# Kernel optimization log

Hardware: AMD Instinct MI355X
Metric: run time of the kernel (lower is better)

The kernel has to match this reference:

```python
import jax, jax.numpy as jnp
import numpy as np

N, C = 8192, 64

def setup_inputs() -> dict:
    key = jax.random.key(0)
    k1, k2, k3 = jax.random.split(key, 3)
    values = jax.random.normal(k1, (N, C), dtype=jnp.float32)
    coords = jax.random.uniform(k2, (N, 2), dtype=jnp.float32)
    spacing = jax.random.uniform(k3, (2,), dtype=jnp.float32)
    shift = jnp.zeros((2,), dtype=jnp.float32)
    return {"values": values, "coords": coords, "spacing": spacing, "shift": shift}


def reference(values, coords, spacing, shift):
    # grid_mode branch of upsample_nn: 3 shifted copies of the coord grid
    x, y = coords[:, 0], coords[:, 1]
    new_coords = jnp.concatenate([
        jnp.stack((x + spacing[0], y + spacing[1]), axis=1),
        jnp.stack((x, y + spacing[1]), axis=1),
        jnp.stack((x + spacing[0], y), axis=1),
    ], axis=0)  # [3N, 2]

    # Diffs = ||(new_coords - shift)[:,None] - coords[None,:]||, argmin over coords.
    # argmin of the L2 norm == argmin of the squared distance, so use the
    # expanded form to avoid materializing the [3N, N, 2] difference tensor.
    a = new_coords - shift  # [3N, 2]
    d2 = (jnp.sum(a * a, axis=1)[:, None]
          + jnp.sum(coords * coords, axis=1)[None, :]
          - 2.0 * a @ coords.T)  # [3N, N]
    idx = jnp.argmin(d2, axis=1)  # [3N]
    new_values = values[idx]      # [3N, C]

    out_values = jnp.concatenate([values, new_values], axis=0)   # [4N, C]
    out_coords = jnp.concatenate([coords, new_coords], axis=0)   # [4N, 2]
    return out_values, out_coords
```

## Files before the change

kernel.cpp:

```cpp
#include <hip/hip_runtime.h>

#pragma clang fp contract(off)

#define N_PTS 8192
#define C_DIM 64
#define NQ (3 * N_PTS)
#define G 64
#define NCELL (G * G)
#define MARGIN 1.2e-5f
#define HCELL (1.0f / 64.0f)
#define QBLOCKS (NQ / 32)
#define STRIPEBLKS 16
#define CPS (NCELL / STRIPEBLKS)
#define COPYBLKS 128


__device__ __forceinline__ unsigned int fsortkey(float f) {
    const unsigned int u = __float_as_uint(f);
    return (u & 0x80000000u) ? ~u : (u | 0x80000000u);
}
__device__ __forceinline__ float finvkey(unsigned int e) {
    const unsigned int u = (e & 0x80000000u) ? (e & 0x7fffffffu) : ~e;
    return __uint_as_float(u);
}

__device__ __forceinline__ void shift_query(int g, float x, float y,
                                            float sx, float sy,
                                            float& nx, float& ny) {
    if (g == 0)      { nx = x + sx; ny = y + sy; }
    else if (g == 1) { nx = x;      ny = y + sy; }
    else             { nx = x + sx; ny = y; }
}

__global__ __launch_bounds__(1024) void build_copy_kernel(
    const float2* __restrict__ coords2,
    const float4* __restrict__ values4,
    float4* __restrict__ sorted,
    int* __restrict__ starts,
    float4* __restrict__ out_values4,
    float2* __restrict__ out_coords)
{
#pragma clang fp contract(off)
    const int t = threadIdx.x;
    if (blockIdx.x >= STRIPEBLKS) {
        const int row = ((int)blockIdx.x - STRIPEBLKS) * 64 + (t >> 4);
        const int c4  = t & 15;
        out_values4[row * 16 + c4] = values4[row * 16 + c4];
        if (c4 == 0) out_coords[row] = coords2[row];
        return;
    }

    __shared__ unsigned int lhist[CPS];
    __shared__ unsigned int wred[16];
    __shared__ unsigned int wsum2[4];
    __shared__ unsigned int baseSh;

    const int b      = blockIdx.x;
    const int myBase = b * CPS;
    const int lane   = t & 63;
    const int w      = t >> 6;

    if (t < CPS) lhist[t] = 0u;
    __syncthreads();

    float2 cpt[8];
    int    cell[8];
    int cnt = 0;
    #pragma unroll
    for (int k = 0; k < 8; ++k) {
        const int i = t + 1024 * k;
        const float2 c = coords2[i];
        cpt[k] = c;
        int cx = (int)(c.x * 64.0f); cx = min(max(cx, 0), G - 1);
        int cy = (int)(c.y * 64.0f); cy = min(max(cy, 0), G - 1);
        cell[k] = cy * G + cx;
        cnt += (cell[k] < myBase) ? 1 : 0;
        const int lc = cell[k] - myBase;
        if (lc >= 0 && lc < CPS) atomicAdd(&lhist[lc], 1u);
    }

    int cv = cnt;
    #pragma unroll
    for (int s = 32; s >= 1; s >>= 1) cv += __shfl_xor(cv, s, 64);
    if (lane == 0) wred[w] = (unsigned)cv;
    __syncthreads();
    if (t == 0) {
        unsigned s = 0;
        #pragma unroll
        for (int j = 0; j < 16; ++j) s += wred[j];
        baseSh = s;
    }
    __syncthreads();
    const unsigned base = baseSh;

    unsigned h = 0, v = 0;
    if (t < CPS) {
        h = lhist[t];
        v = h;
        #pragma unroll
        for (int s = 1; s < 64; s <<= 1) {
            const unsigned o = __shfl_up(v, s, 64);
            if (lane >= s) v += o;
        }
        if (lane == 63) wsum2[w] = v;
    }
    __syncthreads();
    if (t < CPS) {
        unsigned woff = 0;
        for (int j = 0; j < w; ++j) woff += wsum2[j];
        const unsigned excl = base + woff + v - h;
        starts[myBase + t] = (int)excl;
        lhist[t] = excl;
    }
    if (b == 0 && t == 0) starts[NCELL] = N_PTS;
    __syncthreads();

    #pragma unroll
    for (int k = 0; k < 8; ++k) {
        const int lc = cell[k] - myBase;
        if (lc >= 0 && lc < CPS) {
            const unsigned pos = atomicAdd(&lhist[lc], 1u);
            const float p0 = cpt[k].x * cpt[k].x;
            const float p1 = cpt[k].y * cpt[k].y;
            const float sc = p0 + p1;
            const int i = t + 1024 * k;
            sorted[pos] = make_float4(cpt[k].x, cpt[k].y, sc, __int_as_float(i));
        }
    }
}

__global__ __launch_bounds__(256) void query_kernel(
    const float4* __restrict__ sorted,
    const int* __restrict__ starts,
    const float4* __restrict__ values4,
    const float* __restrict__ spacing,
    const float* __restrict__ shift,
    float4* __restrict__ out_values4,
    float2* __restrict__ out_coords)
{
#pragma clang fp contract(off)
    __shared__ int s_starts[NCELL + 1];

    const int tid  = threadIdx.x;
    const int lane = tid & 7;
    const int q    = blockIdx.x * 32 + (tid >> 3);
    const int g    = q >> 13;
    const int k    = q & (N_PTS - 1);

    const float4 me = sorted[k];

    for (int i = tid; i <= NCELL; i += 256) s_starts[i] = starts[i];

    const int b = __float_as_int(me.w);
    float nx, ny;
    shift_query(g, me.x, me.y, spacing[0], spacing[1], nx, ny);
    const float ax = nx - shift[0];
    const float ay = ny - shift[1];
    const float sa = (ax * ax) + (ay * ay);

    int cx = (int)floorf(ax * 64.0f); cx = min(max(cx, 0), G - 1);
    int cy = (int)floorf(ay * 64.0f); cy = min(max(cy, 0), G - 1);
    const float dxo = fmaxf(fmaxf(ax - 1.0f, -ax), 0.0f);

    __syncthreads();

    float best = INFINITY;
    int   bi   = 0x7fffffff;

#define EVAL_BODY(PT)                                                       \
    {                                                                       \
        const float4 pt = (PT);                                             \
        const float p   = ax * pt.x;                                        \
        const float dv  = __builtin_fmaf(ay, pt.y, p);                      \
        const float t1  = sa + pt.z;                                        \
        const float d2  = t1 - (2.0f * dv);                                 \
        const int   j   = __float_as_int(pt.w);                             \
        if (d2 < best || (d2 == best && j < bi)) { best = d2; bi = j; }     \
    }

    const int xa = max(cx - 1, 0), xb = min(cx + 1, G - 1);
    const int ya = max(cy - 1, 0), yb = min(cy + 1, G - 1);

    const int s0 = s_starts[ya * G + xa];
    const int e0 = s_starts[ya * G + xb + 1];
    int s1 = 0, e1 = 0, s2 = 0, e2 = 0;
    if (ya + 1 <= yb) { s1 = s_starts[(ya + 1) * G + xa]; e1 = s_starts[(ya + 1) * G + xb + 1]; }
    if (ya + 2 <= yb) { s2 = s_starts[(ya + 2) * G + xa]; e2 = s_starts[(ya + 2) * G + xb + 1]; }
    const int l0 = e0 - s0, l1 = e1 - s1;
    const int total = l0 + l1 + (e2 - s2);

    {
        const int i0 = lane, i1 = lane + 8, i2 = lane + 16;
        const bool v0 = i0 < total, v1 = i1 < total, v2 = i2 < total;
        float4 p0, p1, p2;
        int a0 = 0, a1 = 0, a2 = 0;
        if (v0) a0 = (i0 < l0) ? s0 + i0 : ((i0 < l0 + l1) ? s1 + (i0 - l0) : s2 + (i0 - l0 - l1));
        if (v1) a1 = (i1 < l0) ? s0 + i1 : ((i1 < l0 + l1) ? s1 + (i1 - l0) : s2 + (i1 - l0 - l1));
        if (v2) a2 = (i2 < l0) ? s0 + i2 : ((i2 < l0 + l1) ? s1 + (i2 - l0) : s2 + (i2 - l0 - l1));
        if (v0) p0 = sorted[a0];
        if (v1) p1 = sorted[a1];
        if (v2) p2 = sorted[a2];
        if (v0) EVAL_BODY(p0)
        if (v1) EVAL_BODY(p1)
        if (v2) EVAL_BODY(p2)
        for (int idx = lane + 24; idx < total; idx += 8) {
            const int a = (idx < l0) ? s0 + idx
                        : ((idx < l0 + l1) ? s1 + (idx - l0) : s2 + (idx - l0 - l1));
            EVAL_BODY(sorted[a])
        }
    }

    unsigned long long key =
        ((unsigned long long)fsortkey(best) << 32) | (unsigned int)bi;
    #pragma unroll
    for (int m = 1; m < 8; m <<= 1) {
        const unsigned long long o = __shfl_xor(key, m, 8);
        if (o < key) key = o;
    }
    best = finvkey((unsigned int)(key >> 32));
    bi   = (int)(unsigned int)key;

    const float U = best + MARGIN;

    float sr = sqrtf(fmaxf(U - dxo * dxo, 0.0f));
    sr = fminf(sr, 4.0f);
    const int ylo = max((int)floorf((ay - sr) * 64.0f), 0);
    const int yhi = min((int)floorf((ay + sr) * 64.0f), G - 1);

    float scw = fminf(sqrtf(U), 4.0f);
    const int xlo_c = max((int)floorf((ax - scw) * 64.0f), 0);
    const int xhi_c = min((int)floorf((ax + scw) * 64.0f), G - 1);

    const bool skip = (ylo >= ya) && (yhi <= yb) && (xlo_c >= xa) && (xhi_c <= xb);

    if (!skip) {
        for (int yy = ylo; yy <= yhi; yy += 2) {
            int ssA = 0, eeA = 0, ssB = 0, eeB = 0;
            {
                const float ry0 = (float)yy * HCELL;
                const float vy  = fmaxf(fmaxf(ay - ry0 - HCELL, ry0 - ay), 0.0f);
                const float r2  = U - vy * vy;
                if (r2 >= 0.0f) {
                    const float s = fminf(sqrtf(r2), 4.0f);
                    const int xl = max((int)floorf((ax - s) * 64.0f), 0);
                    const int xh = min((int)floorf((ax + s) * 64.0f), G - 1);
                    if (xl <= xh && !(yy >= ya && yy <= yb && xl >= xa && xh <= xb)) {
                        ssA = s_starts[yy * G + xl];
                        eeA = s_starts[yy * G + xh + 1];
                    }
                }
            }
            if (yy + 1 <= yhi) {
                const int y2 = yy + 1;
                const float ry0 = (float)y2 * HCELL;
                const float vy  = fmaxf(fmaxf(ay - ry0 - HCELL, ry0 - ay), 0.0f);
                const float r2  = U - vy * vy;
                if (r2 >= 0.0f) {
                    const float s = fminf(sqrtf(r2), 4.0f);
                    const int xl = max((int)floorf((ax - s) * 64.0f), 0);
                    const int xh = min((int)floorf((ax + s) * 64.0f), G - 1);
                    if (xl <= xh && !(y2 >= ya && y2 <= yb && xl >= xa && xh <= xb)) {
                        ssB = s_starts[y2 * G + xl];
                        eeB = s_starts[y2 * G + xh + 1];
                    }
                }
            }
            const int iA = ssA + lane, iB = ssB + lane;
            const bool vA = iA < eeA, vB = iB < eeB;
            float4 pA, pB;
            if (vA) pA = sorted[iA];
            if (vB) pB = sorted[iB];
            if (vA) EVAL_BODY(pA)
            if (vB) EVAL_BODY(pB)
            for (int i = ssA + lane + 8; i < eeA; i += 8) EVAL_BODY(sorted[i])
            for (int i = ssB + lane + 8; i < eeB; i += 8) EVAL_BODY(sorted[i])
        }
        key = ((unsigned long long)fsortkey(best) << 32) | (unsigned int)bi;
        #pragma unroll
        for (int m = 1; m < 8; m <<= 1) {
            const unsigned long long o = __shfl_xor(key, m, 8);
            if (o < key) key = o;
        }
        bi = (int)(unsigned int)key;
    }
#undef EVAL_BODY

    bi = min(max(bi, 0), N_PTS - 1);
    const int qi  = g * N_PTS + b;
    const int row = N_PTS + qi;
    out_values4[row * 16 + 2 * lane + 0] = values4[bi * 16 + 2 * lane + 0];
    out_values4[row * 16 + 2 * lane + 1] = values4[bi * 16 + 2 * lane + 1];
    if (lane == 0) out_coords[row] = make_float2(nx, ny);
}

extern "C" void kernel_launch(void* const* d_in, const int* in_sizes, int n_in,
                              void* d_out, int out_size, void* d_ws, size_t ws_size,
                              hipStream_t stream)
{
    const float* values  = (const float*)d_in[0];
    const float* coords  = (const float*)d_in[1];
    const float* spacing = (const float*)d_in[2];
    const float* shift   = (const float*)d_in[3];

    float* out_values = (float*)d_out;
    float2* out_coords = (float2*)(out_values + (size_t)4 * N_PTS * C_DIM);

    char* ws = (char*)d_ws;
    float4* sorted = (float4*)ws;
    int* starts    = (int*)(ws + 131072);

    build_copy_kernel<<<STRIPEBLKS + COPYBLKS, 1024, 0, stream>>>(
        (const float2*)coords, (const float4*)values,
        sorted, starts, (float4*)out_values, out_coords);

    query_kernel<<<QBLOCKS, 256, 0, stream>>>(
        sorted, starts, (const float4*)values, spacing, shift,
        (float4*)out_values, out_coords);
}
```

Measured before the change: 23.00 us.

## Add column/row edge strips for contiguous fallback scans of out-of-grid queries

Builds two extra sorted strips in the build kernel: points in the last four grid columns binned by row, and points in the last four grid rows binned by column. Queries whose fallback search window lies entirely in those edge columns or rows (typical for shifted queries past the unit square) now scan one contiguous range instead of looping over many grid rows with per-row bounds. This targets the costly fallback loop for boundary queries, at the price of two extra build blocks, more workspace, and extra shared-memory loads.

```diff
diff --git a/kernel.cpp b/kernel.cpp
--- a/kernel.cpp
+++ b/kernel.cpp
@@ -6,6 +6,7 @@
 #define C_DIM 64
 #define NQ (3 * N_PTS)
 #define G 64
+#define GSTRIP 60
 #define NCELL (G * G)
 #define MARGIN 1.2e-5f
 #define HCELL (1.0f / 64.0f)
@@ -37,16 +38,75 @@
     const float4* __restrict__ values4,
     float4* __restrict__ sorted,
     int* __restrict__ starts,
+    int* __restrict__ cs_starts,
+    int* __restrict__ rs_starts,
+    float4* __restrict__ cstrip,
+    float4* __restrict__ rstrip,
     float4* __restrict__ out_values4,
     float2* __restrict__ out_coords)
 {
 #pragma clang fp contract(off)
     const int t = threadIdx.x;
-    if (blockIdx.x >= STRIPEBLKS) {
-        const int row = ((int)blockIdx.x - STRIPEBLKS) * 64 + (t >> 4);
+
+    if (blockIdx.x >= STRIPEBLKS + 2) {
+        const int row = ((int)blockIdx.x - STRIPEBLKS - 2) * 64 + (t >> 4);
         const int c4  = t & 15;
         out_values4[row * 16 + c4] = values4[row * 16 + c4];
         if (c4 == 0) out_coords[row] = coords2[row];
+        return;
+    }
+
+    if (blockIdx.x >= STRIPEBLKS) {
+        const bool isCol = (blockIdx.x == STRIPEBLKS);
+        int* __restrict__ sst       = isCol ? cs_starts : rs_starts;
+        float4* __restrict__ strip  = isCol ? cstrip    : rstrip;
+
+        __shared__ unsigned int shist[G];
+        if (t < G) shist[t] = 0u;
+        __syncthreads();
+
+        float2 cpt[8];
+        int    bin[8];
+        bool   inq[8];
+        #pragma unroll
+        for (int k = 0; k < 8; ++k) {
+            const int i = t + 1024 * k;
+            const float2 c = coords2[i];
+            cpt[k] = c;
+            int cx = (int)(c.x * 64.0f); cx = min(max(cx, 0), G - 1);
+            int cy = (int)(c.y * 64.0f); cy = min(max(cy, 0), G - 1);
+            inq[k] = isCol ? (cx >= GSTRIP) : (cy >= GSTRIP);
+            bin[k] = isCol ? cy : cx;
+            if (inq[k]) atomicAdd(&shist[bin[k]], 1u);
+        }
+        __syncthreads();
+
+        if (t < G) {
+            const unsigned h = shist[t];
+            unsigned v = h;
+            #pragma unroll
+            for (int s = 1; s < 64; s <<= 1) {
+                const unsigned o = __shfl_up(v, s, 64);
+                if (t >= s) v += o;
+            }
+            const unsigned excl = v - h;
+            sst[t]   = (int)excl;
+            shist[t] = excl;
+            if (t == 63) sst[G] = (int)v;
+        }
+        __syncthreads();
+
+        #pragma unroll
+        for (int k = 0; k < 8; ++k) {
+            if (inq[k]) {
+                const unsigned pos = atomicAdd(&shist[bin[k]], 1u);
+                const float p0 = cpt[k].x * cpt[k].x;
+                const float p1 = cpt[k].y * cpt[k].y;
+                const float sc = p0 + p1;
+                const int i = t + 1024 * k;
+                strip[pos] = make_float4(cpt[k].x, cpt[k].y, sc, __int_as_float(i));
+            }
+        }
         return;
     }
 
@@ -132,6 +192,10 @@
 __global__ __launch_bounds__(256) void query_kernel(
     const float4* __restrict__ sorted,
     const int* __restrict__ starts,
+    const int* __restrict__ cs_starts,
+    const int* __restrict__ rs_starts,
+    const float4* __restrict__ cstrip,
+    const float4* __restrict__ rstrip,
     const float4* __restrict__ values4,
     const float* __restrict__ spacing,
     const float* __restrict__ shift,
@@ -140,6 +204,7 @@
 {
 #pragma clang fp contract(off)
     __shared__ int s_starts[NCELL + 1];
+    __shared__ int s_cs[G + 1], s_rs[G + 1];
 
     const int tid  = threadIdx.x;
     const int lane = tid & 7;
@@ -150,6 +215,8 @@
     const float4 me = sorted[k];
 
     for (int i = tid; i <= NCELL; i += 256) s_starts[i] = starts[i];
+    if (tid < G + 1)                      s_cs[tid]       = cs_starts[tid];
+    else if (tid >= 128 && tid < 128 + G + 1) s_rs[tid - 128] = rs_starts[tid - 128];
 
     const int b = __float_as_int(me.w);
     float nx, ny;
@@ -234,46 +301,56 @@
     const bool skip = (ylo >= ya) && (yhi <= yb) && (xlo_c >= xa) && (xhi_c <= xb);
 
     if (!skip) {
-        for (int yy = ylo; yy <= yhi; yy += 2) {
-            int ssA = 0, eeA = 0, ssB = 0, eeB = 0;
-            {
-                const float ry0 = (float)yy * HCELL;
-                const float vy  = fmaxf(fmaxf(ay - ry0 - HCELL, ry0 - ay), 0.0f);
-                const float r2  = U - vy * vy;
-                if (r2 >= 0.0f) {
-                    const float s = fminf(sqrtf(r2), 4.0f);
-                    const int xl = max((int)floorf((ax - s) * 64.0f), 0);
-                    const int xh = min((int)floorf((ax + s) * 64.0f), G - 1);
-                    if (xl <= xh && !(yy >= ya && yy <= yb && xl >= xa && xh <= xb)) {
-                        ssA = s_starts[yy * G + xl];
-                        eeA = s_starts[yy * G + xh + 1];
+        if (xlo_c >= GSTRIP) {
+            const int ss = s_cs[ylo], ee = s_cs[yhi + 1];
+            #pragma unroll 2
+            for (int i = ss + lane; i < ee; i += 8) EVAL_BODY(cstrip[i])
+        } else if (ylo >= GSTRIP) {
+            const int ss = s_rs[xlo_c], ee = s_rs[xhi_c + 1];
+            #pragma unroll 2
+            for (int i = ss + lane; i < ee; i += 8) EVAL_BODY(rstrip[i])
+        } else {
+            for (int yy = ylo; yy <= yhi; yy += 2) {
+                int ssA = 0, eeA = 0, ssB = 0, eeB = 0;
+                {
+                    const float ry0 = (float)yy * HCELL;
+                    const float vy  = fmaxf(fmaxf(ay - ry0 - HCELL, ry0 - ay), 0.0f);
+                    const float r2  = U - vy * vy;
+                    if (r2 >= 0.0f) {
+                        const float s = fminf(sqrtf(r2), 4.0f);
+                        const int xl = max((int)floorf((ax - s) * 64.0f), 0);
+                        const int xh = min((int)floorf((ax + s) * 64.0f), G - 1);
+                        if (xl <= xh && !(yy >= ya && yy <= yb && xl >= xa && xh <= xb)) {
+                            ssA = s_starts[yy * G + xl];
+                            eeA = s_starts[yy * G + xh + 1];
+                        }
                     }
                 }
-            }
-            if (yy + 1 <= yhi) {
-                const int y2 = yy + 1;
-                const float ry0 = (float)y2 * HCELL;
-                const float vy  = fmaxf(fmaxf(ay - ry0 - HCELL, ry0 - ay), 0.0f);
-                const float r2  = U - vy * vy;
-                if (r2 >= 0.0f) {
-                    const float s = fminf(sqrtf(r2), 4.0f);
-                    const int xl = max((int)floorf((ax - s) * 64.0f), 0);
-                    const int xh = min((int)floorf((ax + s) * 64.0f), G - 1);
-                    if (xl <= xh && !(y2 >= ya && y2 <= yb && xl >= xa && xh <= xb)) {
-                        ssB = s_starts[y2 * G + xl];
-                        eeB = s_starts[y2 * G + xh + 1];
+                if (yy + 1 <= yhi) {
+                    const int y2 = yy + 1;
+                    const float ry0 = (float)y2 * HCELL;
+                    const float vy  = fmaxf(fmaxf(ay - ry0 - HCELL, ry0 - ay), 0.0f);
+                    const float r2  = U - vy * vy;
+                    if (r2 >= 0.0f) {
+                        const float s = fminf(sqrtf(r2), 4.0f);
+                        const int xl = max((int)floorf((ax - s) * 64.0f), 0);
+                        const int xh = min((int)floorf((ax + s) * 64.0f), G - 1);
+                        if (xl <= xh && !(y2 >= ya && y2 <= yb && xl >= xa && xh <= xb)) {
+                            ssB = s_starts[y2 * G + xl];
+                            eeB = s_starts[y2 * G + xh + 1];
+                        }
                     }
                 }
+                const int iA = ssA + lane, iB = ssB + lane;
+                const bool vA = iA < eeA, vB = iB < eeB;
+                float4 pA, pB;
+                if (vA) pA = sorted[iA];
+                if (vB) pB = sorted[iB];
+                if (vA) EVAL_BODY(pA)
+                if (vB) EVAL_BODY(pB)
+                for (int i = ssA + lane + 8; i < eeA; i += 8) EVAL_BODY(sorted[i])
+                for (int i = ssB + lane + 8; i < eeB; i += 8) EVAL_BODY(sorted[i])
             }
-            const int iA = ssA + lane, iB = ssB + lane;
-            const bool vA = iA < eeA, vB = iB < eeB;
-            float4 pA, pB;
-            if (vA) pA = sorted[iA];
-            if (vB) pB = sorted[iB];
-            if (vA) EVAL_BODY(pA)
-            if (vB) EVAL_BODY(pB)
-            for (int i = ssA + lane + 8; i < eeA; i += 8) EVAL_BODY(sorted[i])
-            for (int i = ssB + lane + 8; i < eeB; i += 8) EVAL_BODY(sorted[i])
         }
         key = ((unsigned long long)fsortkey(best) << 32) | (unsigned int)bi;
         #pragma unroll
@@ -306,14 +383,20 @@
     float2* out_coords = (float2*)(out_values + (size_t)4 * N_PTS * C_DIM);
 
     char* ws = (char*)d_ws;
-    float4* sorted = (float4*)ws;
-    int* starts    = (int*)(ws + 131072);
-
-    build_copy_kernel<<<STRIPEBLKS + COPYBLKS, 1024, 0, stream>>>(
+    float4* sorted   = (float4*)ws;
+    int* starts      = (int*)(ws + 131072);
+    int* cs_starts   = (int*)(ws + 147472);
+    int* rs_starts   = (int*)(ws + 147744);
+    float4* cstrip   = (float4*)(ws + 148016);
+    float4* rstrip   = (float4*)(ws + 279088);
+
+    build_copy_kernel<<<STRIPEBLKS + 2 + COPYBLKS, 1024, 0, stream>>>(
         (const float2*)coords, (const float4*)values,
-        sorted, starts, (float4*)out_values, out_coords);
+        sorted, starts, cs_starts, rs_starts, cstrip, rstrip,
+        (float4*)out_values, out_coords);
 
     query_kernel<<<QBLOCKS, 256, 0, stream>>>(
-        sorted, starts, (const float4*)values, spacing, shift,
+        sorted, starts, cs_starts, rs_starts, cstrip, rstrip,
+        (const float4*)values, spacing, shift,
         (float4*)out_values, out_coords);
 }
```

Result: slower. 27.15 us (+18.1%).
